# Optimization experiments

Measured on AMD Instinct MI355X. Metric: run time of the kernel, lower is better.

The kernel has to match this reference:

```python
import jax, jax.numpy as jnp
import numpy as np

HIDDEN = 2048
N_HEAD = 16
N_KV_HEAD = 4
HEAD_DIM = HIDDEN // N_HEAD
B, S = 2, 2048


def setup_inputs() -> dict:
    key = jax.random.key(0)
    ks = jax.random.split(key, 10)
    scale = 1.0 / np.sqrt(HIDDEN)
    x = jax.random.normal(ks[0], (B, S, HIDDEN), dtype=jnp.float32)
    # causal additive mask, broadcastable over batch and heads
    causal = jnp.tril(jnp.ones((S, S), dtype=jnp.bool_))
    attention_mask = jnp.where(causal, 0.0, -1e9).astype(jnp.float32)[None, None]
    wq_w = jax.random.uniform(ks[1], (HIDDEN, HIDDEN), jnp.float32, -scale, scale)
    wq_b = jax.random.uniform(ks[2], (HIDDEN,), jnp.float32, -scale, scale)
    wk_w = jax.random.uniform(ks[3], (N_KV_HEAD * HEAD_DIM, HIDDEN), jnp.float32, -scale, scale)
    wk_b = jax.random.uniform(ks[4], (N_KV_HEAD * HEAD_DIM,), jnp.float32, -scale, scale)
    wv_w = jax.random.uniform(ks[5], (N_KV_HEAD * HEAD_DIM, HIDDEN), jnp.float32, -scale, scale)
    wv_b = jax.random.uniform(ks[6], (N_KV_HEAD * HEAD_DIM,), jnp.float32, -scale, scale)
    wo_w = jax.random.uniform(ks[7], (HIDDEN, HIDDEN), jnp.float32, -scale, scale)
    wo_b = jax.random.uniform(ks[8], (HIDDEN,), jnp.float32, -scale, scale)
    return dict(x=x, attention_mask=attention_mask, wq_w=wq_w, wq_b=wq_b,
                wk_w=wk_w, wk_b=wk_b, wv_w=wv_w, wv_b=wv_b, wo_w=wo_w, wo_b=wo_b)


def reference(x, attention_mask, wq_w, wq_b, wk_w, wk_b, wv_w, wv_b, wo_w, wo_b):
    bs, seq_len, _ = x.shape
    group = N_HEAD // N_KV_HEAD
    q = x @ wq_w.T + wq_b  # [B,S,H*D]
    k = x @ wk_w.T + wk_b  # [B,S,Hkv*D]
    v = x @ wv_w.T + wv_b
    q = q.reshape(bs, seq_len, N_HEAD, HEAD_DIM).transpose(0, 2, 1, 3)        # [B,H,S,D]
    k = k.reshape(bs, seq_len, N_KV_HEAD, HEAD_DIM).transpose(0, 2, 1, 3)     # [B,Hkv,S,D]
    v = v.reshape(bs, seq_len, N_KV_HEAD, HEAD_DIM).transpose(0, 2, 1, 3)
    # GQA: share each kv head across `group` query heads (repeat_interleave equiv)
    qg = q.reshape(bs, N_KV_HEAD, group, seq_len, HEAD_DIM)
    scores = jnp.einsum('bkgqd,bkld->bkgql', qg, k) / np.sqrt(HEAD_DIM)       # [B,Hkv,g,S,S]
    scores = scores + attention_mask[:, :, None]  # mask broadcast over head dims
    attn = jax.nn.softmax(scores, axis=-1)  # dropout is identity at inference
    out = jnp.einsum('bkgql,bkld->bkgqd', attn, v)                             # [B,Hkv,g,S,D]
    out = out.reshape(bs, N_HEAD, seq_len, HEAD_DIM).transpose(0, 2, 1, 3)
    out = out.reshape(bs, seq_len, HIDDEN)
    return out @ wo_w.T + wo_b
```

## Files before the change

### kernel.cpp

```cpp
#include <hip/hip_runtime.h>

typedef __bf16 bf16;
typedef __bf16 bf16x8 __attribute__((ext_vector_type(8)));
typedef __bf16 bf16x4 __attribute__((ext_vector_type(4)));
typedef __bf16 bf16x2 __attribute__((ext_vector_type(2)));
typedef float  f32x4  __attribute__((ext_vector_type(4)));

#define HIDDEN 2048
#define NH 16
#define NKV 4
#define HD 128
#define BB 2
#define SS 2048
#define MTOT (BB*SS)
#define KVD (NKV*HD)

__device__ __forceinline__ void gload_lds16(const void* g, void* l) {
  __builtin_amdgcn_global_load_lds(
      (__attribute__((address_space(1))) void*)(void*)g,
      (__attribute__((address_space(3))) void*)l,
      16, 0, 0);
}

__device__ __forceinline__ void pipe_barrier() {
  __builtin_amdgcn_sched_barrier(0);
  __builtin_amdgcn_s_barrier();
  __builtin_amdgcn_sched_barrier(0);
}

__global__ void detect_dtype(const unsigned short* __restrict__ x, int* __restrict__ flag) {
  __shared__ int cnt;
  if (threadIdx.x == 0) cnt = 0;
  __syncthreads();
  int c = 0;
  for (int i = threadIdx.x; i < 8192; i += blockDim.x) {
    float v = fabsf(__uint_as_float((unsigned)x[i] << 16));
    if (v > 64.0f || (v > 0.0f && v < 9.5367431640625e-07f)) ++c;
  }
  atomicAdd(&cnt, c);
  __syncthreads();
  if (threadIdx.x == 0) flag[0] = (cnt > 1024) ? 1 : 0;
}

struct ConvJobs {
  const void* src[8];
  bf16*       dst[8];
  long long   n[8];
};

__device__ __forceinline__ void conv8(const void* src, bf16* dst, long long n,
                                      int f, long long i0, long long stride) {
  const long long n8 = n >> 3;
  if (f) {
    const float4* s4 = (const float4*)src;
    for (long long i = i0; i < n8; i += stride) {
      float4 a = s4[2*i], b = s4[2*i+1];
      bf16x8 o;
      o[0]=(bf16)a.x; o[1]=(bf16)a.y; o[2]=(bf16)a.z; o[3]=(bf16)a.w;
      o[4]=(bf16)b.x; o[5]=(bf16)b.y; o[6]=(bf16)b.z; o[7]=(bf16)b.w;
      *(bf16x8*)&dst[i*8] = o;
    }
  } else {
    const bf16x8* s8 = (const bf16x8*)src;
    for (long long i = i0; i < n8; i += stride)
      *(bf16x8*)&dst[i*8] = s8[i];
  }
}

__global__ void conv_multi(ConvJobs jobs, const int* __restrict__ flag) {
  const int f = flag[0];
  const int a = blockIdx.y;
  conv8(jobs.src[a], jobs.dst[a], jobs.n[a], f,
        (long long)blockIdx.x * blockDim.x + threadIdx.x,
        (long long)gridDim.x * blockDim.x);
}

__global__ void conv_one(const void* __restrict__ src, bf16* __restrict__ dst,
                         long long n, const int* __restrict__ flag) {
  conv8(src, dst, n, flag[0],
        (long long)blockIdx.x * blockDim.x + threadIdx.x,
        (long long)gridDim.x * blockDim.x);
}

__global__ __launch_bounds__(512)
void gemm_qkv256(const bf16* __restrict__ A,
                 const bf16* __restrict__ wq, const bf16* __restrict__ bq,
                 const bf16* __restrict__ wk, const bf16* __restrict__ bk,
                 const bf16* __restrict__ wv, const bf16* __restrict__ bv,
                 bf16* __restrict__ Cq, bf16* __restrict__ Ck, bf16* __restrict__ Cvt)
{
  __shared__ bf16 Asl[2][256*32];
  __shared__ bf16 Bsl[2][256*32];
  const int bid = blockIdx.y * 12 + blockIdx.x;
  const int swz = (bid & 7) * 24 + (bid >> 3);
  const int bx  = swz % 12;
  const int by  = swz / 12;

  const bf16 *Wp, *bias;
  int n0, mode;
  if (bx < 8)       { Wp = wq; bias = bq; n0 = bx*256;      mode = 0; }
  else if (bx < 10) { Wp = wk; bias = bk; n0 = (bx-8)*256;  mode = 1; }
  else              { Wp = wv; bias = bv; n0 = (bx-10)*256; mode = 2; }

  const int tid  = threadIdx.x;
  const int wave = tid >> 6, lane = tid & 63;
  const int g = lane >> 4, l15 = lane & 15;
  const int wr = wave >> 2, wc = wave & 3;
  const int m0 = by * 256;

  f32x4 acc[8][4] = {};

  auto stage4 = [&](int nb, int k0) {
    #pragma unroll
    for (int i = 0; i < 2; ++i) {
      const int cl  = tid + i*512;
      const int row = cl >> 2, ch = cl & 3;
      const int sc  = ch ^ ((row >> 2) & 3);
      gload_lds16(A  + (size_t)(m0 + row)*HIDDEN + k0 + sc*8, &Asl[nb][cl*8]);
      gload_lds16(Wp + (size_t)(n0 + row)*HIDDEN + k0 + sc*8, &Bsl[nb][cl*8]);
    }
  };

  stage4(0, 0);
  asm volatile("s_waitcnt vmcnt(0)" ::: "memory");
  pipe_barrier();

  const int nt = HIDDEN / 32;
  int buf = 0;
  for (int t = 0; t < nt; ++t) {
    bf16x8 af[4], bfr[4];
    #pragma unroll
    for (int mi = 0; mi < 4; ++mi) {
      const int rl = wr*128 + mi*16 + l15;
      const int ch = g ^ ((rl >> 2) & 3);
      af[mi] = *(const bf16x8*)&Asl[buf][rl*32 + ch*8];
    }
    #pragma unroll
    for (int ni = 0; ni < 4; ++ni) {
      const int rl = wc*64 + ni*16 + l15;
      const int ch = g ^ ((rl >> 2) & 3);
      bfr[ni] = *(const bf16x8*)&Bsl[buf][rl*32 + ch*8];
    }
    if (t + 1 < nt) stage4(buf ^ 1, (t + 1) * 32);
    pipe_barrier();
    __builtin_amdgcn_s_setprio(1);
    #pragma unroll
    for (int mi = 0; mi < 4; ++mi)
      #pragma unroll
      for (int ni = 0; ni < 4; ++ni)
        acc[mi][ni] = __builtin_amdgcn_mfma_f32_16x16x32_bf16(af[mi], bfr[ni], acc[mi][ni], 0, 0, 0);
    __builtin_amdgcn_s_setprio(0);
    #pragma unroll
    for (int mi = 0; mi < 4; ++mi) {
      const int rl = wr*128 + 64 + mi*16 + l15;
      const int ch = g ^ ((rl >> 2) & 3);
      af[mi] = *(const bf16x8*)&Asl[buf][rl*32 + ch*8];
    }
    pipe_barrier();
    __builtin_amdgcn_s_setprio(1);
    #pragma unroll
    for (int mi = 0; mi < 4; ++mi)
      #pragma unroll
      for (int ni = 0; ni < 4; ++ni)
        acc[4+mi][ni] = __builtin_amdgcn_mfma_f32_16x16x32_bf16(af[mi], bfr[ni], acc[4+mi][ni], 0, 0, 0);
    __builtin_amdgcn_s_setprio(0);
    __builtin_amdgcn_sched_barrier(0);
    asm volatile("s_waitcnt vmcnt(0)" ::: "memory");
    __builtin_amdgcn_s_barrier();
    __builtin_amdgcn_sched_barrier(0);
    buf ^= 1;
  }

  if (mode == 2) {
    #pragma unroll
    for (int ni = 0; ni < 4; ++ni) {
      const int cc = n0 + wc*64 + ni*16 + l15;
      const float bv2 = (float)bias[cc];
      #pragma unroll
      for (int mi = 0; mi < 8; ++mi) {
        const int row = m0 + wr*128 + mi*16 + g*4;
        bf16x4 o4;
        #pragma unroll
        for (int r = 0; r < 4; ++r) o4[r] = (bf16)(acc[mi][ni][r] + bv2);
        *(bf16x4*)&Cvt[(size_t)cc*MTOT + row] = o4;
      }
    }
  } else {
    bf16* Cb = (mode == 0) ? Cq : Ck;
    const int N = (mode == 0) ? HIDDEN : KVD;
    #pragma unroll
    for (int ni = 0; ni < 4; ++ni) {
      const int col = n0 + wc*64 + ni*16 + l15;
      const float bv2 = (float)bias[col];
      #pragma unroll
      for (int mi = 0; mi < 8; ++mi) {
        const int row = m0 + wr*128 + mi*16 + g*4;
        #pragma unroll
        for (int r = 0; r < 4; ++r)
          Cb[(size_t)(row + r)*N + col] = (bf16)(acc[mi][ni][r] + bv2);
      }
    }
  }
}

__global__ __launch_bounds__(256)
void gemm_bt(const bf16* __restrict__ A, const bf16* __restrict__ W,
             const bf16* __restrict__ bias, void* __restrict__ C,
             int M, int N, int K, const int* __restrict__ flagp)
{
  __shared__ bf16 As[128*32];
  __shared__ bf16 Bs[128*32];
  const int nwg = gridDim.x * gridDim.y;
  const int bid = blockIdx.y * gridDim.x + blockIdx.x;
  const int cpx = nwg >> 3;
  const int swz = (bid & 7) * cpx + (bid >> 3);
  const int bx  = swz % gridDim.x;
  const int by  = swz / gridDim.x;

  const int tid  = threadIdx.x;
  const int wave = tid >> 6, lane = tid & 63;
  const int g = lane >> 4, l15 = lane & 15;
  const int m0 = by * 128, n0 = bx * 128;
  const int wm = (wave >> 1) * 64, wn = (wave & 1) * 64;
  const int srow = lane >> 2;
  const int scol = (lane & 3) * 8;
  f32x4 acc[4][4] = {};

  for (int k0 = 0; k0 < K; k0 += 32) {
    #pragma unroll
    for (int i = 0; i < 2; ++i) {
      const int seg = wave*2 + i;
      const int row = seg*16 + srow;
      gload_lds16(A + (size_t)(m0+row)*K + k0 + scol, &As[row*32 + scol]);
      gload_lds16(W + (size_t)(n0+row)*K + k0 + scol, &Bs[row*32 + scol]);
    }
    asm volatile("s_waitcnt vmcnt(0)" ::: "memory");
    __syncthreads();
    bf16x8 af[4], bfr[4];
    #pragma unroll
    for (int m = 0; m < 4; ++m)
      af[m] = *(const bf16x8*)&As[(wm + m*16 + l15)*32 + g*8];
    #pragma unroll
    for (int n = 0; n < 4; ++n)
      bfr[n] = *(const bf16x8*)&Bs[(wn + n*16 + l15)*32 + g*8];
    #pragma unroll
    for (int m = 0; m < 4; ++m)
      #pragma unroll
      for (int n = 0; n < 4; ++n)
        acc[m][n] = __builtin_amdgcn_mfma_f32_16x16x32_bf16(af[m], bfr[n], acc[m][n], 0, 0, 0);
    __syncthreads();
  }
  const int outf = flagp ? flagp[0] : 0;
  if (outf) {
    float* Cf = (float*)C;
    #pragma unroll
    for (int n = 0; n < 4; ++n) {
      const int col = n0 + wn + n*16 + l15;
      const float bv = (float)bias[col];
      #pragma unroll
      for (int m = 0; m < 4; ++m) {
        const int row = m0 + wm + m*16 + g*4;
        #pragma unroll
        for (int r = 0; r < 4; ++r)
          Cf[(size_t)(row + r)*N + col] = acc[m][n][r] + bv;
      }
    }
  } else {
    bf16* Cb = (bf16*)C;
    #pragma unroll
    for (int n = 0; n < 4; ++n) {
      const int col = n0 + wn + n*16 + l15;
      const float bv = (float)bias[col];
      #pragma unroll
      for (int m = 0; m < 4; ++m) {
        const int row = m0 + wm + m*16 + g*4;
        #pragma unroll
        for (int r = 0; r < 4; ++r)
          Cb[(size_t)(row + r)*N + col] = (bf16)(acc[m][n][r] + bv);
      }
    }
  }
}

#define QB 64
#define PPAD 72

__global__ __launch_bounds__(256)
void attn_fwd(const bf16* __restrict__ Q, const bf16* __restrict__ K,
              const bf16* __restrict__ Vt, bf16* __restrict__ O)
{
  __shared__ bf16 Ks[2][64*128];
  __shared__ bf16 Vs[2][128*64];
  __shared__ bf16 Pl[4][16][PPAD];
  const int tid = threadIdx.x, wave = tid >> 6, lane = tid & 63;
  const int g = lane >> 4, l15 = lane & 15;
  const int bh = blockIdx.y;
  const int b = bh >> 4, h = bh & 15, kvh = h >> 2;
  const bf16* Qh = Q + ((size_t)b*SS)*HIDDEN + h*HD;
  const bf16* Kh = K + ((size_t)b*SS)*KVD + kvh*HD;
  const bf16* Vh = Vt + ((size_t)kvh*HD)*MTOT + (size_t)b*SS;
  bf16*       Oh = O + ((size_t)b*SS)*HIDDEN + h*HD;

  const float KSC    = 0.12751879526563404f;
  const float NEGBIG = -1.0e30f;

  const int krow_st = (lane >> 4);
  const int vrow_st = (lane >> 3);
  const int ksc     = (lane & 15);
  const int vsc     = (lane & 7) ^ (lane >> 3);

  #pragma unroll 1
  for (int pass = 0; pass < 2; ++pass) {
    const int qt = pass ? (31 - (int)blockIdx.x) : (int)blockIdx.x;
    const int qrow0 = qt*QB + wave*16;
    const int qg    = qrow0 + l15;

    bf16x8 bq[4];
    #pragma unroll
    for (int c = 0; c < 4; ++c)
      bq[c] = *(const bf16x8*)(Qh + (size_t)(qrow0 + l15)*HIDDEN + c*32 + g*8);

    f32x4 od[8] = {};
    float m_run = NEGBIG, l_part = 0.f;
    const int ntiles = qt + 1;

    {
      const int kv0 = 0;
      #pragma unroll
      for (int i = 0; i < 4; ++i) {
        const int s = wave*4 + i;
        const int kr = s*4 + krow_st;
        const int kc = ksc ^ (kr & 7);
        gload_lds16(Kh + (size_t)(kv0 + kr)*KVD + kc*8, &Ks[0][s*512 + lane*8]);
        const int vr = s*8 + vrow_st;
        gload_lds16(Vh + (size_t)vr*MTOT + kv0 + vsc*8, &Vs[0][s*512 + lane*8]);
      }
    }
    asm volatile("s_waitcnt vmcnt(0)" ::: "memory");
    __syncthreads();

    int buf = 0;
    #pragma unroll 1
    for (int t = 0; t < ntiles; ++t) {
      const int kv0 = t * 64;

      if (t + 1 < ntiles) {
        const int kv1 = kv0 + 64;
        #pragma unroll
        for (int i = 0; i < 4; ++i) {
          const int s = wave*4 + i;
          const int kr = s*4 + krow_st;
          const int kc = ksc ^ (kr & 7);
          gload_lds16(Kh + (size_t)(kv1 + kr)*KVD + kc*8, &Ks[buf^1][s*512 + lane*8]);
          const int vr = s*8 + vrow_st;
          gload_lds16(Vh + (size_t)vr*MTOT + kv1 + vsc*8, &Vs[buf^1][s*512 + lane*8]);
        }
      }

      f32x4 st[4];
      #pragma unroll
      for (int nb = 0; nb < 4; ++nb) {
        f32x4 s = {};
        #pragma unroll
        for (int c = 0; c < 4; ++c) {
          const int krow = nb*16 + l15;
          const int kch  = (c*4 + g) ^ (krow & 7);
          bf16x8 ka = *(const bf16x8*)&Ks[buf][krow*128 + kch*8];
          s = __builtin_amdgcn_mfma_f32_16x16x32_bf16(ka, bq[c], s, 0, 0, 0);
        }
        st[nb] = s;
      }

      float x[16];
      float mt = NEGBIG;
      if (t == ntiles - 1) {
        #pragma unroll
        for (int nb = 0; nb < 4; ++nb)
          #pragma unroll
          for (int r = 0; r < 4; ++r) {
            const int kv = kv0 + nb*16 + g*4 + r;
            float v = (kv <= qg) ? st[nb][r] : NEGBIG;
            x[nb*4 + r] = v;
            mt = fmaxf(mt, v);
          }
      } else {
        #pragma unroll
        for (int nb = 0; nb < 4; ++nb)
          #pragma unroll
          for (int r = 0; r < 4; ++r) {
            x[nb*4 + r] = st[nb][r];
            mt = fmaxf(mt, st[nb][r]);
          }
      }
      mt = fmaxf(mt, __shfl_xor(mt, 16, 64));
      mt = fmaxf(mt, __shfl_xor(mt, 32, 64));

      if (!__all((mt - m_run) <= 62.0f)) {
        const float m_new = fmaxf(m_run, mt);
        const float corr  = __builtin_amdgcn_exp2f((m_run - m_new) * KSC);
        l_part *= corr;
        #pragma unroll
        for (int db = 0; db < 8; ++db) od[db] *= corr;
        m_run = m_new;
      }

      float psum = 0.f;
      bf16x2 pk[4][2];
      #pragma unroll
      for (int nb = 0; nb < 4; ++nb) {
        const float p0 = __builtin_amdgcn_exp2f((x[nb*4+0] - m_run) * KSC);
        const float p1 = __builtin_amdgcn_exp2f((x[nb*4+1] - m_run) * KSC);
        const float p2 = __builtin_amdgcn_exp2f((x[nb*4+2] - m_run) * KSC);
        const float p3 = __builtin_amdgcn_exp2f((x[nb*4+3] - m_run) * KSC);
        psum += p0 + p1 + p2 + p3;
        pk[nb][0] = bf16x2{(bf16)p0, (bf16)p1};
        pk[nb][1] = bf16x2{(bf16)p2, (bf16)p3};
      }
      l_part += psum;

      #pragma unroll
      for (int nb = 0; nb < 4; ++nb) {
        *(bf16x2*)&Pl[wave][l15][nb*16 + g*4 + 0] = pk[nb][0];
        *(bf16x2*)&Pl[wave][l15][nb*16 + g*4 + 2] = pk[nb][1];
      }
      asm volatile("s_waitcnt lgkmcnt(0)" ::: "memory");
      __builtin_amdgcn_sched_barrier(0);

      #pragma unroll
      for (int c = 0; c < 2; ++c) {
        bf16x8 pb = *(const bf16x8*)&Pl[wave][l15][c*32 + g*8];
        #pragma unroll
        for (int db = 0; db < 8; ++db) {
          const int vrow = db*16 + l15;
          const int vch  = (c*4 + g) ^ (l15 & 7);
          bf16x8 va = *(const bf16x8*)&Vs[buf][vrow*64 + vch*8];
          od[db] = __builtin_amdgcn_mfma_f32_16x16x32_bf16(va, pb, od[db], 0, 0, 0);
        }
      }

      asm volatile("s_waitcnt vmcnt(0)" ::: "memory");
      __syncthreads();
      buf ^= 1;
    }

    float lt = l_part;
    lt += __shfl_xor(lt, 16, 64);
    lt += __shfl_xor(lt, 32, 64);
    const float inv = 1.0f / lt;
    #pragma unroll
    for (int db = 0; db < 8; ++db) {
      bf16x4 o4;
      #pragma unroll
      for (int r = 0; r < 4; ++r) o4[r] = (bf16)(od[db][r] * inv);
      *(bf16x4*)(Oh + (size_t)qg*HIDDEN + db*16 + g*4) = o4;
    }
  }
}

extern "C" void kernel_launch(void* const* d_in, const int* in_sizes, int n_in,
                              void* d_out, int out_size, void* d_ws, size_t ws_size,
                              hipStream_t stream)
{
  (void)in_sizes; (void)n_in; (void)out_size; (void)ws_size;
  const void* x    = d_in[0];
  const void* wq_w = d_in[2];
  const void* wq_b = d_in[3];
  const void* wk_w = d_in[4];
  const void* wk_b = d_in[5];
  const void* wv_w = d_in[6];
  const void* wv_b = d_in[7];
  const void* wo_w = d_in[8];
  const void* wo_b = d_in[9];

  int*  flag = (int*)d_ws;
  bf16* base = (bf16*)((char*)d_ws + 256);
  const long long NX  = (long long)MTOT*HIDDEN;
  const long long NWQ = (long long)HIDDEN*HIDDEN;
  const long long NWK = (long long)KVD*HIDDEN;
  bf16* x_ao = base;
  bf16* wqwo = x_ao + NX;
  bf16* wk_c = wqwo + NWQ;
  bf16* wv_c = wk_c + NWK;
  bf16* bq_c = wv_c + NWK;
  bf16* bk_c = bq_c + 2048;
  bf16* bv_c = bk_c + 512;
  bf16* bo_c = bv_c + 512;
  bf16* q_ws  = bo_c + 2048;
  bf16* k_ws  = q_ws + NX;
  bf16* vt_ws = k_ws + (long long)MTOT*KVD;

  detect_dtype<<<1, 256, 0, stream>>>((const unsigned short*)x, flag);

  ConvJobs jb;
  jb.src[0] = x;    jb.dst[0] = x_ao; jb.n[0] = NX;
  jb.src[1] = wq_w; jb.dst[1] = wqwo; jb.n[1] = NWQ;
  jb.src[2] = wk_w; jb.dst[2] = wk_c; jb.n[2] = NWK;
  jb.src[3] = wv_w; jb.dst[3] = wv_c; jb.n[3] = NWK;
  jb.src[4] = wq_b; jb.dst[4] = bq_c; jb.n[4] = 2048;
  jb.src[5] = wk_b; jb.dst[5] = bk_c; jb.n[5] = 512;
  jb.src[6] = wv_b; jb.dst[6] = bv_c; jb.n[6] = 512;
  jb.src[7] = wo_b; jb.dst[7] = bo_c; jb.n[7] = 2048;
  conv_multi<<<dim3(512, 8), 256, 0, stream>>>(jb, flag);

  gemm_qkv256<<<dim3(12, MTOT/256), 512, 0, stream>>>(x_ao, wqwo, bq_c, wk_c, bk_c,
                                                      wv_c, bv_c, q_ws, k_ws, vt_ws);

  conv_one<<<dim3(512), 256, 0, stream>>>(wo_w, wqwo, NWQ, flag);

  attn_fwd<<<dim3(16, BB*NH), 256, 0, stream>>>(q_ws, k_ws, vt_ws, x_ao);

  gemm_bt<<<dim3(HIDDEN/128, MTOT/128), 256, 0, stream>>>(x_ao, wqwo, bo_c, d_out, MTOT, HIDDEN, HIDDEN, flag);
}
```

Baseline: 232.4 us.

## Triple-buffer QKV GEMM loads and merge paired causal attention tiles into 8-wave blocks

Result: no change. 231.1 us (-0.6%).

```diff
diff --git a/kernel.cpp b/kernel.cpp
--- a/kernel.cpp
+++ b/kernel.cpp
@@ -20,12 +20,6 @@
       (__attribute__((address_space(1))) void*)(void*)g,
       (__attribute__((address_space(3))) void*)l,
       16, 0, 0);
-}
-
-__device__ __forceinline__ void pipe_barrier() {
-  __builtin_amdgcn_sched_barrier(0);
-  __builtin_amdgcn_s_barrier();
-  __builtin_amdgcn_sched_barrier(0);
 }
 
 __global__ void detect_dtype(const unsigned short* __restrict__ x, int* __restrict__ flag) {
@@ -89,8 +83,8 @@
                  const bf16* __restrict__ wv, const bf16* __restrict__ bv,
                  bf16* __restrict__ Cq, bf16* __restrict__ Ck, bf16* __restrict__ Cvt)
 {
-  __shared__ bf16 Asl[2][256*32];
-  __shared__ bf16 Bsl[2][256*32];
+  __shared__ bf16 Asl[3][256*32];
+  __shared__ bf16 Bsl[3][256*32];
   const int bid = blockIdx.y * 12 + blockIdx.x;
   const int swz = (bid & 7) * 24 + (bid >> 3);
   const int bx  = swz % 12;
@@ -122,27 +116,27 @@
   };
 
   stage4(0, 0);
-  asm volatile("s_waitcnt vmcnt(0)" ::: "memory");
-  pipe_barrier();
+  stage4(1, 32);
+  asm volatile("s_waitcnt vmcnt(4)" ::: "memory");
+  __builtin_amdgcn_s_barrier();
 
   const int nt = HIDDEN / 32;
-  int buf = 0;
+  int c0 = 0, c1 = 1, c2 = 2;
   for (int t = 0; t < nt; ++t) {
+    if (t + 2 < nt) stage4(c2, (t + 2) * 32);
     bf16x8 af[4], bfr[4];
     #pragma unroll
     for (int mi = 0; mi < 4; ++mi) {
       const int rl = wr*128 + mi*16 + l15;
       const int ch = g ^ ((rl >> 2) & 3);
-      af[mi] = *(const bf16x8*)&Asl[buf][rl*32 + ch*8];
+      af[mi] = *(const bf16x8*)&Asl[c0][rl*32 + ch*8];
     }
     #pragma unroll
     for (int ni = 0; ni < 4; ++ni) {
       const int rl = wc*64 + ni*16 + l15;
       const int ch = g ^ ((rl >> 2) & 3);
-      bfr[ni] = *(const bf16x8*)&Bsl[buf][rl*32 + ch*8];
-    }
-    if (t + 1 < nt) stage4(buf ^ 1, (t + 1) * 32);
-    pipe_barrier();
+      bfr[ni] = *(const bf16x8*)&Bsl[c0][rl*32 + ch*8];
+    }
     __builtin_amdgcn_s_setprio(1);
     #pragma unroll
     for (int mi = 0; mi < 4; ++mi)
@@ -154,9 +148,8 @@
     for (int mi = 0; mi < 4; ++mi) {
       const int rl = wr*128 + 64 + mi*16 + l15;
       const int ch = g ^ ((rl >> 2) & 3);
-      af[mi] = *(const bf16x8*)&Asl[buf][rl*32 + ch*8];
-    }
-    pipe_barrier();
+      af[mi] = *(const bf16x8*)&Asl[c0][rl*32 + ch*8];
+    }
     __builtin_amdgcn_s_setprio(1);
     #pragma unroll
     for (int mi = 0; mi < 4; ++mi)
@@ -165,10 +158,11 @@
         acc[4+mi][ni] = __builtin_amdgcn_mfma_f32_16x16x32_bf16(af[mi], bfr[ni], acc[4+mi][ni], 0, 0, 0);
     __builtin_amdgcn_s_setprio(0);
     __builtin_amdgcn_sched_barrier(0);
-    asm volatile("s_waitcnt vmcnt(0)" ::: "memory");
+    if (t + 2 < nt) { asm volatile("s_waitcnt vmcnt(4)" ::: "memory"); }
+    else            { asm volatile("s_waitcnt vmcnt(0)" ::: "memory"); }
     __builtin_amdgcn_s_barrier();
     __builtin_amdgcn_sched_barrier(0);
-    buf ^= 1;
+    const int tmp = c0; c0 = c1; c1 = c2; c2 = tmp;
   }
 
   if (mode == 2) {
@@ -282,16 +276,15 @@
   }
 }
 
-#define QB 64
 #define PPAD 72
 
-__global__ __launch_bounds__(256)
+__global__ __launch_bounds__(512)
 void attn_fwd(const bf16* __restrict__ Q, const bf16* __restrict__ K,
               const bf16* __restrict__ Vt, bf16* __restrict__ O)
 {
   __shared__ bf16 Ks[2][64*128];
-  __shared__ bf16 Vs[2][128*64];
-  __shared__ bf16 Pl[4][16][PPAD];
+  __shared__ bf16 Vs[128*64];
+  __shared__ bf16 Pl[8][16][PPAD];
   const int tid = threadIdx.x, wave = tid >> 6, lane = tid & 63;
   const int g = lane >> 4, l15 = lane & 15;
   const int bh = blockIdx.y;
@@ -304,60 +297,54 @@
   const float KSC    = 0.12751879526563404f;
   const float NEGBIG = -1.0e30f;
 
-  const int krow_st = (lane >> 4);
-  const int vrow_st = (lane >> 3);
-  const int ksc     = (lane & 15);
-  const int vsc     = (lane & 7) ^ (lane >> 3);
-
+  const int x      = blockIdx.x;
+  const int qtB    = 31 - x;
+  const int qtMine = (wave < 4) ? x : qtB;
+  const int qrow0  = qtMine*64 + (wave & 3)*16;
+  const int qg     = qrow0 + l15;
+
+  bf16x8 bq[4];
+  #pragma unroll
+  for (int c = 0; c < 4; ++c)
+    bq[c] = *(const bf16x8*)(Qh + (size_t)(qrow0 + l15)*HIDDEN + c*32 + g*8);
+
+  f32x4 od[8] = {};
+  float m_run = NEGBIG, l_part = 0.f;
+
+  auto stageK = [&](int bi, int kv0) {
+    #pragma unroll
+    for (int i = 0; i < 2; ++i) {
+      const int seg = wave*2 + i;
+      const int kr  = seg*4 + (lane >> 4);
+      const int kc  = (lane & 15) ^ (kr & 7);
+      gload_lds16(Kh + (size_t)(kv0 + kr)*KVD + kc*8, &Ks[bi][seg*512 + lane*8]);
+    }
+  };
+  auto stageV = [&](int kv0) {
+    #pragma unroll
+    for (int i = 0; i < 2; ++i) {
+      const int seg = wave*2 + i;
+      const int vr  = seg*8 + (lane >> 3);
+      const int vc  = (lane & 7) ^ (lane >> 3);
+      gload_lds16(Vh + (size_t)vr*MTOT + kv0 + vc*8, &Vs[seg*512 + lane*8]);
+    }
+  };
+
+  stageK(0, 0);
+  asm volatile("s_waitcnt vmcnt(0)" ::: "memory");
+  __builtin_amdgcn_s_barrier();
+
+  int buf = 0;
   #pragma unroll 1
-  for (int pass = 0; pass < 2; ++pass) {
-    const int qt = pass ? (31 - (int)blockIdx.x) : (int)blockIdx.x;
-    const int qrow0 = qt*QB + wave*16;
-    const int qg    = qrow0 + l15;
-
-    bf16x8 bq[4];
-    #pragma unroll
-    for (int c = 0; c < 4; ++c)
-      bq[c] = *(const bf16x8*)(Qh + (size_t)(qrow0 + l15)*HIDDEN + c*32 + g*8);
-
-    f32x4 od[8] = {};
-    float m_run = NEGBIG, l_part = 0.f;
-    const int ntiles = qt + 1;
-
-    {
-      const int kv0 = 0;
-      #pragma unroll
-      for (int i = 0; i < 4; ++i) {
-        const int s = wave*4 + i;
-        const int kr = s*4 + krow_st;
-        const int kc = ksc ^ (kr & 7);
-        gload_lds16(Kh + (size_t)(kv0 + kr)*KVD + kc*8, &Ks[0][s*512 + lane*8]);
-        const int vr = s*8 + vrow_st;
-        gload_lds16(Vh + (size_t)vr*MTOT + kv0 + vsc*8, &Vs[0][s*512 + lane*8]);
-      }
-    }
-    asm volatile("s_waitcnt vmcnt(0)" ::: "memory");
-    __syncthreads();
-
-    int buf = 0;
-    #pragma unroll 1
-    for (int t = 0; t < ntiles; ++t) {
-      const int kv0 = t * 64;
-
-      if (t + 1 < ntiles) {
-        const int kv1 = kv0 + 64;
-        #pragma unroll
-        for (int i = 0; i < 4; ++i) {
-          const int s = wave*4 + i;
-          const int kr = s*4 + krow_st;
-          const int kc = ksc ^ (kr & 7);
-          gload_lds16(Kh + (size_t)(kv1 + kr)*KVD + kc*8, &Ks[buf^1][s*512 + lane*8]);
-          const int vr = s*8 + vrow_st;
-          gload_lds16(Vh + (size_t)vr*MTOT + kv1 + vsc*8, &Vs[buf^1][s*512 + lane*8]);
-        }
-      }
-
+  for (int t = 0; t <= qtB; ++t) {
+    const int kv0 = t * 64;
+    stageV(kv0);
+    if (t < qtB) stageK(buf ^ 1, kv0 + 64);
+
+    const bool active = (t <= qtMine);
+    if (active) {
       f32x4 st[4];
+      __builtin_amdgcn_s_setprio(1);
       #pragma unroll
       for (int nb = 0; nb < 4; ++nb) {
         f32x4 s = {};
@@ -370,17 +357,18 @@
         }
         st[nb] = s;
       }
-
-      float x[16];
+      __builtin_amdgcn_s_setprio(0);
+
+      float xx[16];
       float mt = NEGBIG;
-      if (t == ntiles - 1) {
+      if (t == qtMine) {
         #pragma unroll
         for (int nb = 0; nb < 4; ++nb)
           #pragma unroll
           for (int r = 0; r < 4; ++r) {
             const int kv = kv0 + nb*16 + g*4 + r;
             float v = (kv <= qg) ? st[nb][r] : NEGBIG;
-            x[nb*4 + r] = v;
+            xx[nb*4 + r] = v;
             mt = fmaxf(mt, v);
           }
       } else {
@@ -388,7 +376,7 @@
         for (int nb = 0; nb < 4; ++nb)
           #pragma unroll
           for (int r = 0; r < 4; ++r) {
-            x[nb*4 + r] = st[nb][r];
+            xx[nb*4 + r] = st[nb][r];
             mt = fmaxf(mt, st[nb][r]);
           }
       }
@@ -408,10 +396,10 @@
       bf16x2 pk[4][2];
       #pragma unroll
       for (int nb = 0; nb < 4; ++nb) {
-        const float p0 = __builtin_amdgcn_exp2f((x[nb*4+0] - m_run) * KSC);
-        const float p1 = __builtin_amdgcn_exp2f((x[nb*4+1] - m_run) * KSC);
-        const float p2 = __builtin_amdgcn_exp2f((x[nb*4+2] - m_run) * KSC);
-        const float p3 = __builtin_amdgcn_exp2f((x[nb*4+3] - m_run) * KSC);
+        const float p0 = __builtin_amdgcn_exp2f((xx[nb*4+0] - m_run) * KSC);
+        const float p1 = __builtin_amdgcn_exp2f((xx[nb*4+1] - m_run) * KSC);
+        const float p2 = __builtin_amdgcn_exp2f((xx[nb*4+2] - m_run) * KSC);
+        const float p3 = __builtin_amdgcn_exp2f((xx[nb*4+3] - m_run) * KSC);
         psum += p0 + p1 + p2 + p3;
         pk[nb][0] = bf16x2{(bf16)p0, (bf16)p1};
         pk[nb][1] = bf16x2{(bf16)p2, (bf16)p3};
@@ -423,9 +411,16 @@
         *(bf16x2*)&Pl[wave][l15][nb*16 + g*4 + 0] = pk[nb][0];
         *(bf16x2*)&Pl[wave][l15][nb*16 + g*4 + 2] = pk[nb][1];
       }
+    }
+
+    if (t < qtB) { asm volatile("s_waitcnt vmcnt(2)" ::: "memory"); }
+    else         { asm volatile("s_waitcnt vmcnt(0)" ::: "memory"); }
+    __builtin_amdgcn_s_barrier();
+
+    if (active) {
       asm volatile("s_waitcnt lgkmcnt(0)" ::: "memory");
       __builtin_amdgcn_sched_barrier(0);
-
+      __builtin_amdgcn_s_setprio(1);
       #pragma unroll
       for (int c = 0; c < 2; ++c) {
         bf16x8 pb = *(const bf16x8*)&Pl[wave][l15][c*32 + g*8];
@@ -433,27 +428,28 @@
         for (int db = 0; db < 8; ++db) {
           const int vrow = db*16 + l15;
           const int vch  = (c*4 + g) ^ (l15 & 7);
-          bf16x8 va = *(const bf16x8*)&Vs[buf][vrow*64 + vch*8];
+          bf16x8 va = *(const bf16x8*)&Vs[vrow*64 + vch*8];
           od[db] = __builtin_amdgcn_mfma_f32_16x16x32_bf16(va, pb, od[db], 0, 0, 0);
         }
       }
-
-      asm volatile("s_waitcnt vmcnt(0)" ::: "memory");
-      __syncthreads();
-      buf ^= 1;
-    }
-
-    float lt = l_part;
-    lt += __shfl_xor(lt, 16, 64);
-    lt += __shfl_xor(lt, 32, 64);
-    const float inv = 1.0f / lt;
-    #pragma unroll
-    for (int db = 0; db < 8; ++db) {
-      bf16x4 o4;
-      #pragma unroll
-      for (int r = 0; r < 4; ++r) o4[r] = (bf16)(od[db][r] * inv);
-      *(bf16x4*)(Oh + (size_t)qg*HIDDEN + db*16 + g*4) = o4;
-    }
+      __builtin_amdgcn_s_setprio(0);
+    }
+
+    asm volatile("s_waitcnt vmcnt(0)" ::: "memory");
+    __builtin_amdgcn_s_barrier();
+    buf ^= 1;
+  }
+
+  float lt = l_part;
+  lt += __shfl_xor(lt, 16, 64);
+  lt += __shfl_xor(lt, 32, 64);
+  const float inv = 1.0f / lt;
+  #pragma unroll
+  for (int db = 0; db < 8; ++db) {
+    bf16x4 o4;
+    #pragma unroll
+    for (int r = 0; r < 4; ++r) o4[r] = (bf16)(od[db][r] * inv);
+    *(bf16x4*)(Oh + (size_t)qg*HIDDEN + db*16 + g*4) = o4;
   }
 }
 
@@ -507,7 +503,7 @@
 
   conv_one<<<dim3(512), 256, 0, stream>>>(wo_w, wqwo, NWQ, flag);
 
-  attn_fwd<<<dim3(16, BB*NH), 256, 0, stream>>>(q_ws, k_ws, vt_ws, x_ao);
+  attn_fwd<<<dim3(16, BB*NH), 512, 0, stream>>>(q_ws, k_ws, vt_ws, x_ao);
 
   gemm_bt<<<dim3(HIDDEN/128, MTOT/128), 256, 0, stream>>>(x_ao, wqwo, bo_c, d_out, MTOT, HIDDEN, HIDDEN, flag);
 }
```
